# Kernel tuning notes

Measured on AMD Instinct MI355X. Metric: run time of the kernel, lower is better.

The kernel has to match this reference:

```python
import jax, jax.numpy as jnp
import numpy as np

FEATURES, NEURONS, THETA, TAU, H = 128, 512, 256, 1.0, 0.1
B, T = 64, 2048

def setup_inputs() -> dict:
    key = jax.random.key(0)
    ks = jax.random.split(key, 8)
    IN = FEATURES + NEURONS
    s = lambda n: 1.0 / np.sqrt(n)
    return {
        "I": jax.random.normal(ks[0], (B, T, FEATURES), dtype=jnp.float32),
        "W_ih": jax.random.uniform(ks[1], (THETA, IN), jnp.float32, -s(THETA), s(THETA)),
        "W_hh": jax.random.uniform(ks[2], (THETA, THETA), jnp.float32, -s(THETA), s(THETA)),
        "b_ih": jax.random.uniform(ks[3], (THETA,), jnp.float32, -s(THETA), s(THETA)),
        "b_hh": jax.random.uniform(ks[4], (THETA,), jnp.float32, -s(THETA), s(THETA)),
        "W_out": jax.random.uniform(ks[5], (NEURONS, THETA), jnp.float32, -s(THETA), s(THETA)),
        "b_out": jax.random.uniform(ks[6], (NEURONS,), jnp.float32, -s(THETA), s(THETA)),
        "A": jax.random.normal(ks[7], (NEURONS,), dtype=jnp.float32),
    }

def reference(I, W_ih, W_hh, b_ih, b_hh, W_out, b_out, A):
    batch = I.shape[0]
    x0 = jnp.zeros((batch, NEURONS), I.dtype)
    s0 = jnp.zeros((batch, THETA), I.dtype)

    def step(carry, I_t):
        x, s = carry
        cat = jnp.concatenate([x, I_t], axis=-1)            # [B, neurons+features]
        s_new = jnp.tanh(cat @ W_ih.T + b_ih + s @ W_hh.T + b_hh)  # single-step tanh RNN
        f = jax.nn.relu(s_new @ W_out.T + b_out)            # [B, neurons]
        # implicit-Euler ODE update
        x_next = (x + H * (f * A)) / (1.0 + H * (1.0 / TAU + f))
        return (x_next, s_new), x_next

    _, xs = jax.lax.scan(step, (x0, s0), jnp.swapaxes(I, 0, 1))  # [T, B, neurons]
    return jnp.swapaxes(xs, 0, 1)  # [B, T, neurons]
```

## Files before the change

kernel.cpp:

```cpp
#include <hip/hip_runtime.h>
#include <hip/hip_bf16.h>

#define TT 2048
typedef unsigned int uint32;
typedef unsigned long long uint64;

#define WREG_N   (4 * 88 * 512)
#define EXA_N    (2 * 64 * 4 * 256)

__device__ __forceinline__ float lo16(uint32 u) { return __uint_as_float(u << 16); }
__device__ __forceinline__ float hi16(uint32 u) { return __uint_as_float(u & 0xffff0000u); }

__device__ __forceinline__ uint32 packbf(float lo, float hi)
{
    __hip_bfloat16 a = __float2bfloat16(lo), b = __float2bfloat16(hi);
    unsigned short ua = *reinterpret_cast<unsigned short*>(&a);
    unsigned short ub = *reinterpret_cast<unsigned short*>(&b);
    return (uint32)ua | ((uint32)ub << 16);
}

__device__ __forceinline__ float getA(const float* W_ih, const float* W_hh,
                                      int g, int j, int k)
{
    if (k < 128) return W_ih[j * 640 + 128 * g + k];
    if (k < 192) return W_hh[j * 256 + 64 * g + (k - 128)];
    return W_ih[j * 640 + 512 + 32 * g + (k - 192)];
}

__global__ void prep_kernel(const float* __restrict__ W_ih,
                            const float* __restrict__ W_hh,
                            const float* __restrict__ W_out,
                            uint32* __restrict__ WREG,
                            uint64* __restrict__ exA)
{
    int idx = blockIdx.x * blockDim.x + threadIdx.x;
    if (idx < WREG_N) {
        int tid = idx & 511;
        int q   = idx >> 9;
        int g   = q / 88;
        int i   = q % 88;
        float lo, hi;
        if (i < 56) {
            int j = tid >> 1, h = tid & 1;
            int k0 = 112 * h + 2 * i;
            lo = getA(W_ih, W_hh, g, j, k0);
            hi = getA(W_ih, W_hh, g, j, k0 + 1);
        } else {
            int p  = i - 56;
            int s  = p >> 1, qq = p & 1;
            int kq = tid & 3;
            int n  = 128 * g + (tid >> 2);
            int blk = (s + 2 * kq) & 15;
            int k0  = 64 * kq + 4 * blk + 2 * qq;
            lo = W_out[n * 256 + k0];
            hi = W_out[n * 256 + k0 + 1];
        }
        WREG[idx] = packbf(lo, hi);
    } else if (idx < WREG_N + EXA_N) {
        exA[idx - WREG_N] = 0ULL;
    }
}

__device__ __forceinline__ void bar_lds()
{
    asm volatile("s_waitcnt lgkmcnt(0)" ::: "memory");
    __builtin_amdgcn_s_barrier();
    asm volatile("" ::: "memory");
}

__global__ __launch_bounds__(512)
void scan_kernel(const float* __restrict__ I,
                 const float* __restrict__ b_ih, const float* __restrict__ b_hh,
                 const float* __restrict__ b_out, const float* __restrict__ A,
                 const uint32* __restrict__ WREG,
                 uint64* exA,
                 float* __restrict__ out)
{
    __shared__ float4 aloc4[2][56];
    __shared__ float  sful[256];

    const int tid = threadIdx.x;
    const int bid = blockIdx.x;
    const int b   = bid & 63;
    const int g   = bid >> 6;

    uint32 wA[56], wB[32];
    const uint32* wsrc = WREG + (g * 88) * 512 + tid;
    #pragma unroll
    for (int i = 0; i < 56; ++i) wA[i] = wsrc[i * 512];
    #pragma unroll
    for (int i = 0; i < 32; ++i) wB[i] = wsrc[(56 + i) * 512];

    const int h  = tid & 1;
    const int jA = tid >> 1;
    const int kq = tid & 3;
    const int nB = tid >> 2;

    const float bs   = ((tid & 1) == 0) ? (b_ih[jA] + b_hh[jA]) : 0.f;
    const float bo_r = ((tid & 3) == 0) ? b_out[128 * g + nB] : 0.f;
    const float Av_r = ((tid & 3) == 0) ? A[128 * g + nB] : 0.f;

    const size_t iBase   = (size_t)b * TT * 128 + 32 * g;
    const size_t outBase = (size_t)b * TT * 512 + 128 * g;

    {
        float* a0 = (float*)&aloc4[0][0];
        if (tid < 192) a0[tid] = 0.f;
        else if (tid < 224) a0[tid] = I[iBase + (tid - 192)];
    }
    __syncthreads();

    for (int t = 0; t < TT; ++t) {
        const int par = t & 1;
        const float4* rd = aloc4[par];
        float*        wr = (float*)aloc4[par ^ 1];

        float iv = 0.f;
        if (tid < 32) {
            int tl = (t + 1 < TT) ? (t + 1) : t;
            iv = I[iBase + (size_t)tl * 128 + tid];
        }

        float a0 = 0.f, a1 = 0.f;
        #pragma unroll
        for (int i = 0; i < 28; ++i) {
            float4 av = rd[28 * h + i];
            uint32 w0 = wA[2 * i], w1 = wA[2 * i + 1];
            a0 = fmaf(av.x, lo16(w0), a0);
            a1 = fmaf(av.y, hi16(w0), a1);
            a0 = fmaf(av.z, lo16(w1), a0);
            a1 = fmaf(av.w, hi16(w1), a1);
        }
        float accA = a0 + a1;
        accA += __shfl_xor(accA, 1);

        const uint32 tgt = (uint32)(t + 1);
        uint64* ex = exA + (size_t)(par * 64 + b) * (4 * 256);

        if ((tid & 1) == 0) {
            uint64 u = ((uint64)tgt << 32) | (uint64)__float_as_uint(accA);
            __hip_atomic_store(ex + g * 256 + jA, u,
                               __ATOMIC_RELAXED, __HIP_MEMORY_SCOPE_AGENT);

            float v0 = 0.f, v1 = 0.f, v2 = 0.f;
            uint32 got = 0;
            const int g1 = (g + 1) & 3, g2 = (g + 2) & 3, g3 = (g + 3) & 3;
            do {
                if (!(got & 1u)) {
                    uint64 u1 = __hip_atomic_load(ex + g1 * 256 + jA,
                                                  __ATOMIC_RELAXED, __HIP_MEMORY_SCOPE_AGENT);
                    if ((uint32)(u1 >> 32) == tgt) { v0 = __uint_as_float((uint32)u1); got |= 1u; }
                }
                if (!(got & 2u)) {
                    uint64 u2 = __hip_atomic_load(ex + g2 * 256 + jA,
                                                  __ATOMIC_RELAXED, __HIP_MEMORY_SCOPE_AGENT);
                    if ((uint32)(u2 >> 32) == tgt) { v1 = __uint_as_float((uint32)u2); got |= 2u; }
                }
                if (!(got & 4u)) {
                    uint64 u3 = __hip_atomic_load(ex + g3 * 256 + jA,
                                                  __ATOMIC_RELAXED, __HIP_MEMORY_SCOPE_AGENT);
                    if ((uint32)(u3 >> 32) == tgt) { v2 = __uint_as_float((uint32)u3); got |= 4u; }
                }
            } while (got != 7u);

            float pre = accA + bs + v0 + v1 + v2;
            float e  = __expf(2.f * pre);
            float sn = 1.f - 2.f / (e + 1.f);
            sful[jA] = sn;
            int d = jA - 64 * g;
            if (d >= 0 && d < 64) wr[128 + d] = sn;
        }
        bar_lds();

        const float4* s4 = (const float4*)sful;
        float c0 = 0.f, c1 = 0.f;
        #pragma unroll
        for (int s2 = 0; s2 < 16; ++s2) {
            int blk = (s2 + 2 * kq) & 15;
            float4 sv = s4[16 * kq + blk];
            uint32 w0 = wB[2 * s2], w1 = wB[2 * s2 + 1];
            c0 = fmaf(sv.x, lo16(w0), c0);
            c1 = fmaf(sv.y, hi16(w0), c1);
            c0 = fmaf(sv.z, lo16(w1), c0);
            c1 = fmaf(sv.w, hi16(w1), c1);
        }
        float f = c0 + c1;
        f += __shfl_xor(f, 1);
        f += __shfl_xor(f, 2);

        if ((tid & 3) == 0) {
            float ff = fmaxf(f + bo_r, 0.f);
            float xo = ((const float*)rd)[nB];
            float xn = (xo + 0.1f * ff * Av_r) / (1.1f + 0.1f * ff);
            wr[nB] = xn;
            out[outBase + (size_t)t * 512 + nB] = xn;
        }
        if (tid < 32) wr[192 + tid] = iv;
        bar_lds();
    }
}

extern "C" void kernel_launch(void* const* d_in, const int* in_sizes, int n_in,
                              void* d_out, int out_size, void* d_ws, size_t ws_size,
                              hipStream_t stream)
{
    const float* I     = (const float*)d_in[0];
    const float* W_ih  = (const float*)d_in[1];
    const float* W_hh  = (const float*)d_in[2];
    const float* b_ih  = (const float*)d_in[3];
    const float* b_hh  = (const float*)d_in[4];
    const float* W_out = (const float*)d_in[5];
    const float* b_out = (const float*)d_in[6];
    const float* A     = (const float*)d_in[7];

    uint32* WREG = (uint32*)d_ws;
    uint64* exA  = (uint64*)((uint32*)d_ws + WREG_N);

    const int total = WREG_N + EXA_N;
    prep_kernel<<<(total + 1023) / 1024, 1024, 0, stream>>>(W_ih, W_hh, W_out, WREG, exA);
    scan_kernel<<<256, 512, 0, stream>>>(I, b_ih, b_hh, b_out, A,
                                         WREG, exA, (float*)d_out);
}
```

Measured before the change: 4.420 ms.

## Use sc0 L2-coherent fast exchange path with probe and fp32 register weights

Adds a second exchange buffer that is written and polled with raw sc0 global loads and stores, so cross-block state exchange hits the shared L2 instead of going through the slower agent-scope atomic path. A startup handshake between the four blocks of each batch row checks that the fast path actually sees peer writes, and the code falls back to the atomic buffer if it does not or if a poll times out. Weights are also kept as fp32 in registers instead of packed bf16, which removes unpack instructions and raises register use to 176 per thread, and launch bounds now request 2 blocks per CU. The risks are register spills, extra stores each step, and depending on sc0 coherence across CUs.

```diff
diff --git a/kernel.cpp b/kernel.cpp
--- a/kernel.cpp
+++ b/kernel.cpp
@@ -5,19 +5,9 @@
 typedef unsigned int uint32;
 typedef unsigned long long uint64;
 
-#define WREG_N   (4 * 88 * 512)
+#define WREGF_N  (4 * 176 * 512)
 #define EXA_N    (2 * 64 * 4 * 256)
-
-__device__ __forceinline__ float lo16(uint32 u) { return __uint_as_float(u << 16); }
-__device__ __forceinline__ float hi16(uint32 u) { return __uint_as_float(u & 0xffff0000u); }
-
-__device__ __forceinline__ uint32 packbf(float lo, float hi)
-{
-    __hip_bfloat16 a = __float2bfloat16(lo), b = __float2bfloat16(hi);
-    unsigned short ua = *reinterpret_cast<unsigned short*>(&a);
-    unsigned short ub = *reinterpret_cast<unsigned short*>(&b);
-    return (uint32)ua | ((uint32)ub << 16);
-}
+#define ZQ_N     (2 * EXA_N + 256)
 
 __device__ __forceinline__ float getA(const float* W_ih, const float* W_hh,
                                       int g, int j, int k)
@@ -30,34 +20,31 @@
 __global__ void prep_kernel(const float* __restrict__ W_ih,
                             const float* __restrict__ W_hh,
                             const float* __restrict__ W_out,
-                            uint32* __restrict__ WREG,
-                            uint64* __restrict__ exA)
+                            float* __restrict__ WREGF,
+                            uint64* __restrict__ zbase)
 {
     int idx = blockIdx.x * blockDim.x + threadIdx.x;
-    if (idx < WREG_N) {
+    if (idx < WREGF_N) {
         int tid = idx & 511;
         int q   = idx >> 9;
-        int g   = q / 88;
-        int i   = q % 88;
-        float lo, hi;
-        if (i < 56) {
+        int g   = q / 176;
+        int i   = q % 176;
+        float v;
+        if (i < 112) {
             int j = tid >> 1, h = tid & 1;
-            int k0 = 112 * h + 2 * i;
-            lo = getA(W_ih, W_hh, g, j, k0);
-            hi = getA(W_ih, W_hh, g, j, k0 + 1);
+            v = getA(W_ih, W_hh, g, j, 112 * h + i);
         } else {
-            int p  = i - 56;
-            int s  = p >> 1, qq = p & 1;
+            int p  = i - 112;
+            int s2 = p >> 2, c = p & 3;
             int kq = tid & 3;
             int n  = 128 * g + (tid >> 2);
-            int blk = (s + 2 * kq) & 15;
-            int k0  = 64 * kq + 4 * blk + 2 * qq;
-            lo = W_out[n * 256 + k0];
-            hi = W_out[n * 256 + k0 + 1];
-        }
-        WREG[idx] = packbf(lo, hi);
-    } else if (idx < WREG_N + EXA_N) {
-        exA[idx - WREG_N] = 0ULL;
+            int blk = (s2 + 2 * kq) & 15;
+            int k   = 64 * kq + 4 * blk + c;
+            v = W_out[n * 256 + k];
+        }
+        WREGF[idx] = v;
+    } else if (idx < WREGF_N + ZQ_N) {
+        zbase[idx - WREGF_N] = 0ULL;
     }
 }
 
@@ -68,35 +55,70 @@
     asm volatile("" ::: "memory");
 }
 
-__global__ __launch_bounds__(512)
+__device__ __forceinline__ void st64_sc0(uint64* p, uint64 v)
+{
+    asm volatile("global_store_dwordx2 %0, %1, off sc0" :: "v"(p), "v"(v) : "memory");
+}
+__device__ __forceinline__ void ld3_64_sc0(const uint64* p1, const uint64* p2,
+                                           const uint64* p3,
+                                           uint64& r1, uint64& r2, uint64& r3)
+{
+    asm volatile("global_load_dwordx2 %0, %3, off sc0\n\t"
+                 "global_load_dwordx2 %1, %4, off sc0\n\t"
+                 "global_load_dwordx2 %2, %5, off sc0\n\t"
+                 "s_waitcnt vmcnt(0)"
+                 : "=&v"(r1), "=&v"(r2), "=&v"(r3)
+                 : "v"(p1), "v"(p2), "v"(p3)
+                 : "memory");
+}
+__device__ __forceinline__ void st32_sc0(uint32* p, uint32 v)
+{
+    asm volatile("global_store_dword %0, %1, off sc0" :: "v"(p), "v"(v) : "memory");
+}
+__device__ __forceinline__ void ld3_32_sc0(const uint32* p1, const uint32* p2,
+                                           const uint32* p3,
+                                           uint32& r1, uint32& r2, uint32& r3)
+{
+    asm volatile("global_load_dword %0, %3, off sc0\n\t"
+                 "global_load_dword %1, %4, off sc0\n\t"
+                 "global_load_dword %2, %5, off sc0\n\t"
+                 "s_waitcnt vmcnt(0)"
+                 : "=&v"(r1), "=&v"(r2), "=&v"(r3)
+                 : "v"(p1), "v"(p2), "v"(p3)
+                 : "memory");
+}
+
+__global__ __launch_bounds__(512, 2)
 void scan_kernel(const float* __restrict__ I,
                  const float* __restrict__ b_ih, const float* __restrict__ b_hh,
                  const float* __restrict__ b_out, const float* __restrict__ A,
-                 const uint32* __restrict__ WREG,
-                 uint64* exA,
+                 const float* __restrict__ WREGF,
+                 uint64* exS, uint64* exF, uint32* pv,
                  float* __restrict__ out)
 {
     __shared__ float4 aloc4[2][56];
     __shared__ float  sful[256];
+    __shared__ int    l2flag;
 
     const int tid = threadIdx.x;
     const int bid = blockIdx.x;
     const int b   = bid & 63;
     const int g   = bid >> 6;
-
-    uint32 wA[56], wB[32];
-    const uint32* wsrc = WREG + (g * 88) * 512 + tid;
+    const int g1  = (g + 1) & 3, g2 = (g + 2) & 3, g3 = (g + 3) & 3;
+
+    float wAf[112], wBf[64];
+    const float* wsrc = WREGF + (g * 176) * 512 + tid;
     #pragma unroll
-    for (int i = 0; i < 56; ++i) wA[i] = wsrc[i * 512];
+    for (int i = 0; i < 112; ++i) wAf[i] = wsrc[i * 512];
     #pragma unroll
-    for (int i = 0; i < 32; ++i) wB[i] = wsrc[(56 + i) * 512];
+    for (int i = 0; i < 64; ++i)  wBf[i] = wsrc[(112 + i) * 512];
 
     const int h  = tid & 1;
     const int jA = tid >> 1;
     const int kq = tid & 3;
     const int nB = tid >> 2;
 
-    const float bs   = ((tid & 1) == 0) ? (b_ih[jA] + b_hh[jA]) : 0.f;
+    const float bs   = b_ih[jA] + b_hh[jA];
     const float bo_r = ((tid & 3) == 0) ? b_out[128 * g + nB] : 0.f;
     const float Av_r = ((tid & 3) == 0) ? A[128 * g + nB] : 0.f;
 
@@ -104,11 +126,40 @@
     const size_t outBase = (size_t)b * TT * 512 + 128 * g;
 
     {
-        float* a0 = (float*)&aloc4[0][0];
-        if (tid < 192) a0[tid] = 0.f;
-        else if (tid < 224) a0[tid] = I[iBase + (tid - 192)];
+        float* a0p = (float*)&aloc4[0][0];
+        if (tid < 192) a0p[tid] = 0.f;
+        else if (tid < 224) a0p[tid] = I[iBase + (tid - 192)];
+    }
+
+    if (tid == 0) {
+        uint32* pb = pv + b * 4;
+        uint32* vt = pv + 256 + b * 4;
+        const uint32 TOK = 0x5EED0001u;
+        st32_sc0(pb + g, TOK);
+        uint32 seen = 0;
+        for (int it = 0; it < 4096 && seen != 7u; ++it) {
+            uint32 r1, r2, r3;
+            ld3_32_sc0(pb + g1, pb + g2, pb + g3, r1, r2, r3);
+            if (r1 == TOK) seen |= 1u;
+            if (r2 == TOK) seen |= 2u;
+            if (r3 == TOK) seen |= 4u;
+        }
+        __hip_atomic_store(vt + g, (seen == 7u) ? 2u : 1u,
+                           __ATOMIC_RELAXED, __HIP_MEMORY_SCOPE_AGENT);
+        uint32 v0, v1, v2, v3;
+        do {
+            v0 = __hip_atomic_load(vt + 0, __ATOMIC_RELAXED, __HIP_MEMORY_SCOPE_AGENT);
+            v1 = __hip_atomic_load(vt + 1, __ATOMIC_RELAXED, __HIP_MEMORY_SCOPE_AGENT);
+            v2 = __hip_atomic_load(vt + 2, __ATOMIC_RELAXED, __HIP_MEMORY_SCOPE_AGENT);
+            v3 = __hip_atomic_load(vt + 3, __ATOMIC_RELAXED, __HIP_MEMORY_SCOPE_AGENT);
+        } while (v0 == 0u || v1 == 0u || v2 == 0u || v3 == 0u);
+        l2flag = (v0 == 2u && v1 == 2u && v2 == 2u && v3 == 2u);
     }
     __syncthreads();
+    const bool l2m = (l2flag != 0);
+    bool fastok = l2m;
+
+    const float4* s4 = (const float4*)sful;
 
     for (int t = 0; t < TT; ++t) {
         const int par = t & 1;
@@ -125,45 +176,52 @@
         #pragma unroll
         for (int i = 0; i < 28; ++i) {
             float4 av = rd[28 * h + i];
-            uint32 w0 = wA[2 * i], w1 = wA[2 * i + 1];
-            a0 = fmaf(av.x, lo16(w0), a0);
-            a1 = fmaf(av.y, hi16(w0), a1);
-            a0 = fmaf(av.z, lo16(w1), a0);
-            a1 = fmaf(av.w, hi16(w1), a1);
+            a0 = fmaf(av.x, wAf[4 * i + 0], a0);
+            a1 = fmaf(av.y, wAf[4 * i + 1], a1);
+            a0 = fmaf(av.z, wAf[4 * i + 2], a0);
+            a1 = fmaf(av.w, wAf[4 * i + 3], a1);
         }
         float accA = a0 + a1;
         accA += __shfl_xor(accA, 1);
 
         const uint32 tgt = (uint32)(t + 1);
-        uint64* ex = exA + (size_t)(par * 64 + b) * (4 * 256);
+        const size_t sb  = (size_t)(par * 64 + b) * (4 * 256);
 
         if ((tid & 1) == 0) {
             uint64 u = ((uint64)tgt << 32) | (uint64)__float_as_uint(accA);
-            __hip_atomic_store(ex + g * 256 + jA, u,
+            if (l2m) st64_sc0(exF + sb + g * 256 + jA, u);
+            __hip_atomic_store(exS + sb + g * 256 + jA, u,
                                __ATOMIC_RELAXED, __HIP_MEMORY_SCOPE_AGENT);
 
-            float v0 = 0.f, v1 = 0.f, v2 = 0.f;
+            const uint64* f1 = exF + sb + g1 * 256 + jA;
+            const uint64* f2 = exF + sb + g2 * 256 + jA;
+            const uint64* f3 = exF + sb + g3 * 256 + jA;
+            const uint64* s1 = exS + sb + g1 * 256 + jA;
+            const uint64* s2p = exS + sb + g2 * 256 + jA;
+            const uint64* s3 = exS + sb + g3 * 256 + jA;
+
+            float v0f = 0.f, v1f = 0.f, v2f = 0.f;
             uint32 got = 0;
-            const int g1 = (g + 1) & 3, g2 = (g + 2) & 3, g3 = (g + 3) & 3;
-            do {
-                if (!(got & 1u)) {
-                    uint64 u1 = __hip_atomic_load(ex + g1 * 256 + jA,
-                                                  __ATOMIC_RELAXED, __HIP_MEMORY_SCOPE_AGENT);
-                    if ((uint32)(u1 >> 32) == tgt) { v0 = __uint_as_float((uint32)u1); got |= 1u; }
+            if (fastok) {
+                for (int it = 0; it < 8192 && got != 7u; ++it) {
+                    uint64 u1, u2, u3;
+                    ld3_64_sc0(f1, f2, f3, u1, u2, u3);
+                    if (!(got & 1u) && (uint32)(u1 >> 32) == tgt) { v0f = __uint_as_float((uint32)u1); got |= 1u; }
+                    if (!(got & 2u) && (uint32)(u2 >> 32) == tgt) { v1f = __uint_as_float((uint32)u2); got |= 2u; }
+                    if (!(got & 4u) && (uint32)(u3 >> 32) == tgt) { v2f = __uint_as_float((uint32)u3); got |= 4u; }
                 }
-                if (!(got & 2u)) {
-                    uint64 u2 = __hip_atomic_load(ex + g2 * 256 + jA,
-                                                  __ATOMIC_RELAXED, __HIP_MEMORY_SCOPE_AGENT);
-                    if ((uint32)(u2 >> 32) == tgt) { v1 = __uint_as_float((uint32)u2); got |= 2u; }
-                }
-                if (!(got & 4u)) {
-                    uint64 u3 = __hip_atomic_load(ex + g3 * 256 + jA,
-                                                  __ATOMIC_RELAXED, __HIP_MEMORY_SCOPE_AGENT);
-                    if ((uint32)(u3 >> 32) == tgt) { v2 = __uint_as_float((uint32)u3); got |= 4u; }
-                }
-            } while (got != 7u);
-
-            float pre = accA + bs + v0 + v1 + v2;
+                if (got != 7u) fastok = false;
+            }
+            while (got != 7u) {
+                uint64 u1 = __hip_atomic_load(s1,  __ATOMIC_RELAXED, __HIP_MEMORY_SCOPE_AGENT);
+                uint64 u2 = __hip_atomic_load(s2p, __ATOMIC_RELAXED, __HIP_MEMORY_SCOPE_AGENT);
+                uint64 u3 = __hip_atomic_load(s3,  __ATOMIC_RELAXED, __HIP_MEMORY_SCOPE_AGENT);
+                if (!(got & 1u) && (uint32)(u1 >> 32) == tgt) { v0f = __uint_as_float((uint32)u1); got |= 1u; }
+                if (!(got & 2u) && (uint32)(u2 >> 32) == tgt) { v1f = __uint_as_float((uint32)u2); got |= 2u; }
+                if (!(got & 4u) && (uint32)(u3 >> 32) == tgt) { v2f = __uint_as_float((uint32)u3); got |= 4u; }
+            }
+
+            float pre = accA + bs + v0f + v1f + v2f;
             float e  = __expf(2.f * pre);
             float sn = 1.f - 2.f / (e + 1.f);
             sful[jA] = sn;
@@ -172,17 +230,15 @@
         }
         bar_lds();
 
-        const float4* s4 = (const float4*)sful;
         float c0 = 0.f, c1 = 0.f;
         #pragma unroll
-        for (int s2 = 0; s2 < 16; ++s2) {
-            int blk = (s2 + 2 * kq) & 15;
+        for (int s2i = 0; s2i < 16; ++s2i) {
+            int blk = (s2i + 2 * kq) & 15;
             float4 sv = s4[16 * kq + blk];
-            uint32 w0 = wB[2 * s2], w1 = wB[2 * s2 + 1];
-            c0 = fmaf(sv.x, lo16(w0), c0);
-            c1 = fmaf(sv.y, hi16(w0), c1);
-            c0 = fmaf(sv.z, lo16(w1), c0);
-            c1 = fmaf(sv.w, hi16(w1), c1);
+            c0 = fmaf(sv.x, wBf[4 * s2i + 0], c0);
+            c1 = fmaf(sv.y, wBf[4 * s2i + 1], c1);
+            c0 = fmaf(sv.z, wBf[4 * s2i + 2], c0);
+            c1 = fmaf(sv.w, wBf[4 * s2i + 3], c1);
         }
         float f = c0 + c1;
         f += __shfl_xor(f, 1);
@@ -213,11 +269,15 @@
     const float* b_out = (const float*)d_in[6];
     const float* A     = (const float*)d_in[7];
 
-    uint32* WREG = (uint32*)d_ws;
-    uint64* exA  = (uint64*)((uint32*)d_ws + WREG_N);
-
-    const int total = WREG_N + EXA_N;
-    prep_kernel<<<(total + 1023) / 1024, 1024, 0, stream>>>(W_ih, W_hh, W_out, WREG, exA);
+    float*  WREGF = (float*)d_ws;
+    uint64* zbase = (uint64*)(WREGF + WREGF_N);
+    uint64* exS   = zbase;
+    uint64* exF   = zbase + EXA_N;
+    uint32* pvp   = (uint32*)(zbase + 2 * EXA_N);
+
+    const int total = WREGF_N + ZQ_N;
+    prep_kernel<<<(total + 1023) / 1024, 1024, 0, stream>>>(W_ih, W_hh, W_out,
+                                                            WREGF, zbase);
     scan_kernel<<<256, 512, 0, stream>>>(I, b_ih, b_hh, b_out, A,
-                                         WREG, exA, (float*)d_out);
-}
+                                         WREGF, exS, exF, pvp, (float*)d_out);
+}
```

Result: slower. 8.219 ms (+86.0%).
